# Performance work log

Measured on AMD Instinct MI355X. Metric: run time of the kernel, lower is better.

Reference implementation:

```python
import jax, jax.numpy as jnp
import numpy as np

N_NODES = 12800
N_EDGES = 204800
DIM = 16
EDGE_DIM = 4
NUM_FEAT = 3


def setup_inputs() -> dict:
    key = jax.random.key(0)
    ks = jax.random.split(key, 16)
    s = 0.1
    return {
        "x": jax.random.normal(ks[0], (N_NODES, NUM_FEAT), jnp.float32),
        "edge_index": jax.random.randint(ks[1], (2, N_EDGES), 0, N_NODES, jnp.int32),
        "edge_attr": jax.random.uniform(ks[2], (N_EDGES, EDGE_DIM), jnp.float32),
        "lin0_w": jax.random.normal(ks[3], (DIM, NUM_FEAT), jnp.float32) * s,
        "lin0_b": jax.random.normal(ks[4], (DIM,), jnp.float32) * s,
        "nn1_w": jax.random.normal(ks[5], (DIM, EDGE_DIM), jnp.float32) * s,
        "nn1_b": jax.random.normal(ks[6], (DIM,), jnp.float32) * s,
        "nn2_w": jax.random.normal(ks[7], (DIM * DIM, DIM), jnp.float32) * s,
        "nn2_b": jax.random.normal(ks[8], (DIM * DIM,), jnp.float32) * s,
        "conv_root": jax.random.normal(ks[9], (DIM, DIM), jnp.float32) * s,
        "conv_bias": jax.random.normal(ks[10], (DIM,), jnp.float32) * s,
        "gru_w_ih": jax.random.normal(ks[11], (3 * DIM, DIM), jnp.float32) * s,
        "gru_w_hh": jax.random.normal(ks[12], (3 * DIM, DIM), jnp.float32) * s,
        "gru_b_ih": jax.random.normal(ks[13], (3 * DIM,), jnp.float32) * s,
        "gru_b_hh": jax.random.normal(ks[14], (3 * DIM,), jnp.float32) * s,
    }


def _forward(x, edge_index, edge_attr, lin0_w, lin0_b, nn1_w, nn1_b, nn2_w, nn2_b,
             conv_root, conv_bias, gru_w_ih, gru_w_hh, gru_b_ih, gru_b_hh):
    n = x.shape[0]
    dim = lin0_w.shape[0]
    src, dst = edge_index[0], edge_index[1]

    # edge-conditioned weight matrices, shared across the 6 rounds: [E, dim, dim]
    e_hidden = jax.nn.relu(edge_attr @ nn1_w.T + nn1_b)
    edge_w = (e_hidden @ nn2_w.T + nn2_b).reshape(-1, dim, dim)

    # in-degree for mean aggregation (0 -> divide by 1, result stays 0)
    deg = jax.ops.segment_sum(jnp.ones_like(dst, dtype=x.dtype), dst, num_segments=n)
    inv_deg = (1.0 / jnp.maximum(deg, 1.0))[:, None]

    out = jax.nn.relu(x @ lin0_w.T + lin0_b)  # [N, dim]
    h = out
    for _ in range(6):
        # gather -> per-edge matmul -> scatter-mean
        msg = jnp.einsum('ed,edk->ek', out[src], edge_w)  # [E, dim]
        aggr = jax.ops.segment_sum(msg, dst, num_segments=n) * inv_deg
        m = jax.nn.relu(aggr + out @ conv_root + conv_bias)
        # single GRU step (seq_len = 1)
        gi = m @ gru_w_ih.T + gru_b_ih  # [N, 3*dim]
        gh = h @ gru_w_hh.T + gru_b_hh
        i_r, i_z, i_n = jnp.split(gi, 3, axis=-1)
        h_r, h_z, h_n = jnp.split(gh, 3, axis=-1)
        r = jax.nn.sigmoid(i_r + h_r)
        z = jax.nn.sigmoid(i_z + h_z)
        nhat = jnp.tanh(i_n + r * h_n)
        h = (1.0 - z) * nhat + z * h
        out = h
    return out


def reference(x, edge_index, edge_attr, lin0_w, lin0_b, nn1_w, nn1_b, nn2_w, nn2_b,
              conv_root, conv_bias, gru_w_ih, gru_w_hh, gru_b_ih, gru_b_hh):
    return _forward(x, edge_index, edge_attr, lin0_w, lin0_b, nn1_w, nn1_b, nn2_w,
                    nn2_b, conv_root, conv_bias, gru_w_ih, gru_w_hh, gru_b_ih, gru_b_hh)
```

## Files before the change

### kernel.cpp

```cpp
#include <hip/hip_runtime.h>

#define NN 12800
#define NE 204800
#define BCAP 64
#define NPB 50
#define RTHR (NPB * 16)

#define OFF_W2 0
#define OFF_CR 4416
#define OFF_WI 4736
#define OFF_WH 5696
#define OFF_CB 6656
#define OFF_BI 6672
#define OFF_BH 6720
#define PACKN  6768

__device__ __align__(16) float g_outA[NN * 16];
__device__ __align__(16) float g_outB[NN * 16];
__device__ __align__(16) float g_ehsB[NN * BCAP * 16];
__device__ __align__(16) int g_srcB[NN * BCAP];
__device__ int g_cnt[NN];
__device__ int g_perm[NN];
__device__ __align__(16) float g_wpack[PACKN];

__global__ __launch_bounds__(256) void k_setup(const int* __restrict__ ei,
                                               const float* __restrict__ x,
                                               const float* __restrict__ lw,
                                               const float* __restrict__ lb,
                                               const float* __restrict__ attr,
                                               const float* __restrict__ w1,
                                               const float* __restrict__ b1,
                                               const float* __restrict__ nn2_w,
                                               const float* __restrict__ nn2_b,
                                               const float* __restrict__ cr,
                                               const float* __restrict__ cb,
                                               const float* __restrict__ wi,
                                               const float* __restrict__ wh,
                                               const float* __restrict__ bi,
                                               const float* __restrict__ bh) {
    int gid = blockIdx.x * 256 + threadIdx.x;

    if (blockIdx.x == 0) {
        int tt = threadIdx.x;
        for (int i = tt; i < 4096; i += 256)
            g_wpack[OFF_W2 + (i & 15) * 276 + ((i >> 4) & 15) * 16 + (i >> 8)] = nn2_w[i];
        g_wpack[OFF_W2 + (tt >> 4) * 276 + 256 + (tt & 15)] = nn2_b[tt];
        g_wpack[OFF_CR + (tt & 15) * 20 + (tt >> 4)] = cr[tt];
        for (int i = tt; i < 768; i += 256) {
            g_wpack[OFF_WI + (i >> 4) * 20 + (i & 15)] = wi[i];
            g_wpack[OFF_WH + (i >> 4) * 20 + (i & 15)] = wh[i];
        }
        if (tt < 16) g_wpack[OFF_CB + tt] = cb[tt];
        if (tt < 48) { g_wpack[OFF_BI + tt] = bi[tt]; g_wpack[OFF_BH + tt] = bh[tt]; }
    }

    if (gid < NN) {
        int n = gid;
        float x0 = x[n * 3 + 0], x1 = x[n * 3 + 1], x2 = x[n * 3 + 2];
        float v[16];
#pragma unroll
        for (int j = 0; j < 16; ++j) {
            float t = lb[j] + x0 * lw[j * 3 + 0] + x1 * lw[j * 3 + 1] + x2 * lw[j * 3 + 2];
            v[j] = fmaxf(t, 0.0f);
        }
#pragma unroll
        for (int j = 0; j < 16; j += 4)
            *(float4*)(g_outA + n * 16 + j) = make_float4(v[j], v[j + 1], v[j + 2], v[j + 3]);
    }

    int e = gid;
    int s = ei[e], d = ei[NE + e];
    float4 a = *(const float4*)(attr + e * 4);
    float v[16];
#pragma unroll
    for (int j = 0; j < 16; ++j) {
        float t = b1[j] + a.x * w1[j * 4 + 0] + a.y * w1[j * 4 + 1] +
                  a.z * w1[j * 4 + 2] + a.w * w1[j * 4 + 3];
        v[j] = fmaxf(t, 0.0f);
    }
    int pos = atomicAdd(&g_cnt[d], 1);
    if (pos < BCAP) {
        int slot = d * BCAP + pos;
        g_srcB[slot] = s;
#pragma unroll
        for (int j = 0; j < 16; j += 4)
            *(float4*)(g_ehsB + slot * 16 + j) = make_float4(v[j], v[j + 1], v[j + 2], v[j + 3]);
    }
}

__global__ __launch_bounds__(1024) void k_perm() {
    __shared__ int hist[64];
    int t = threadIdx.x;
    if (t < 64) hist[t] = 0;
    __syncthreads();
    for (int n = t; n < NN; n += 1024)
        atomicAdd(&hist[min(g_cnt[n], 63)], 1);
    __syncthreads();
    if (t < 64) {
        int v = hist[t];
        int incl = v;
#pragma unroll
        for (int off = 1; off < 64; off <<= 1) {
            int u = __shfl_up(incl, off, 64);
            if (t >= off) incl += u;
        }
        hist[t] = incl - v;
    }
    __syncthreads();
    for (int n = t; n < NN; n += 1024) {
        int s = atomicAdd(&hist[min(g_cnt[n], 63)], 1);
        int blk, grp;
        if (s < 12288) {
            int c = s >> 2, r = s & 3;
            blk = c & 255;
            grp = ((c >> 8) << 2) + r;
        } else {
            int l = s - 12288;
            blk = l & 255;
            grp = 48 + (l >> 8);
        }
        g_perm[blk * NPB + grp] = n;
    }
}

__global__ __launch_bounds__(RTHR) void k_round(float* __restrict__ out_final,
                                                int flip, int last) {
    __shared__ __align__(16) float s_pack[PACKN];
    int t = threadIdx.x;
    {
        const float4* srcp = (const float4*)g_wpack;
        float4* dstp = (float4*)s_pack;
        for (int idx = t; idx < PACKN / 4; idx += RTHR) dstp[idx] = srcp[idx];
    }
    __syncthreads();

    const float* s_W2  = s_pack + OFF_W2;
    const float* s_crT = s_pack + OFF_CR;
    const float* s_wi  = s_pack + OFF_WI;
    const float* s_wh  = s_pack + OFF_WH;
    const float* s_cb  = s_pack + OFF_CB;
    const float* s_bi  = s_pack + OFF_BI;
    const float* s_bh  = s_pack + OFF_BH;

    const float* cur = flip ? g_outB : g_outA;
    float*       nxt = flip ? g_outA : g_outB;

    const int grp = t >> 4, j = t & 15;
    const int n = min(max(g_perm[blockIdx.x * NPB + grp], 0), NN - 1);
    int deg = min(g_cnt[n], BCAP);
    if (last && j == 0) g_cnt[n] = 0;
    const int base = n * BCAP;

    float Gd[16];
#pragma unroll
    for (int d = 0; d < 16; ++d) Gd[d] = 0.0f;
    float r16 = 0.0f;
#pragma unroll 4
    for (int q = 0; q < deg; ++q) {
        int slot = base + q;
        int s = min(g_srcB[slot], NN - 1);
        const float* orow = cur + s * 16;
        float ej = g_ehsB[slot * 16 + j];
        float4 o0 = *(const float4*)(orow + 0);
        float4 o1 = *(const float4*)(orow + 4);
        float4 o2 = *(const float4*)(orow + 8);
        float4 o3 = *(const float4*)(orow + 12);
        Gd[0]  += ej * o0.x; Gd[1]  += ej * o0.y; Gd[2]  += ej * o0.z; Gd[3]  += ej * o0.w;
        Gd[4]  += ej * o1.x; Gd[5]  += ej * o1.y; Gd[6]  += ej * o1.z; Gd[7]  += ej * o1.w;
        Gd[8]  += ej * o2.x; Gd[9]  += ej * o2.y; Gd[10] += ej * o2.z; Gd[11] += ej * o2.w;
        Gd[12] += ej * o3.x; Gd[13] += ej * o3.y; Gd[14] += ej * o3.z; Gd[15] += ej * o3.w;
        r16 += orow[j];
    }

    const float* wj = s_W2 + j * 276;
    float part[16];
#pragma unroll
    for (int kp = 0; kp < 16; ++kp) {
        const float* w = wj + kp * 16;
        float4 w0 = *(const float4*)(w + 0);
        float4 w1 = *(const float4*)(w + 4);
        float4 w2 = *(const float4*)(w + 8);
        float4 w3 = *(const float4*)(w + 12);
        part[kp] = Gd[0] * w0.x + Gd[1] * w0.y + Gd[2] * w0.z + Gd[3] * w0.w
                 + Gd[4] * w1.x + Gd[5] * w1.y + Gd[6] * w1.z + Gd[7] * w1.w
                 + Gd[8] * w2.x + Gd[9] * w2.y + Gd[10] * w2.z + Gd[11] * w2.w
                 + Gd[12] * w3.x + Gd[13] * w3.y + Gd[14] * w3.z + Gd[15] * w3.w;
    }
    {
        float4 b0 = *(const float4*)(wj + 256);
        float4 b1 = *(const float4*)(wj + 260);
        float4 b2v = *(const float4*)(wj + 264);
        float4 b3 = *(const float4*)(wj + 268);
        part[0] += r16 * b0.x;  part[1] += r16 * b0.y;  part[2] += r16 * b0.z;  part[3] += r16 * b0.w;
        part[4] += r16 * b1.x;  part[5] += r16 * b1.y;  part[6] += r16 * b1.z;  part[7] += r16 * b1.w;
        part[8] += r16 * b2v.x; part[9] += r16 * b2v.y; part[10] += r16 * b2v.z; part[11] += r16 * b2v.w;
        part[12] += r16 * b3.x; part[13] += r16 * b3.y; part[14] += r16 * b3.z; part[15] += r16 * b3.w;
    }

    float w8[8];
#pragma unroll
    for (int i = 0; i < 8; ++i) {
        int keep = 2 * i + (j & 1);
        w8[i] = part[keep] + __shfl_xor(part[keep ^ 1], 1);
    }
    float w4[4];
#pragma unroll
    for (int i = 0; i < 4; ++i) {
        int keep = 2 * i + ((j >> 1) & 1);
        w4[i] = w8[keep] + __shfl_xor(w8[keep ^ 1], 2);
    }
    float w2[2];
#pragma unroll
    for (int i = 0; i < 2; ++i) {
        int keep = 2 * i + ((j >> 2) & 1);
        w2[i] = w4[keep] + __shfl_xor(w4[keep ^ 1], 4);
    }
    float aggr;
    {
        int keep = (j >> 3) & 1;
        aggr = w2[keep] + __shfl_xor(w2[keep ^ 1], 8);
    }
    float invd = 1.0f / (float)(deg > 0 ? deg : 1);
    float a_k = aggr * invd;
    const int k = j;

    const float* nrow = cur + n * 16;
    float4 q0 = *(const float4*)(nrow + 0);
    float4 q1 = *(const float4*)(nrow + 4);
    float4 q2 = *(const float4*)(nrow + 8);
    float4 q3 = *(const float4*)(nrow + 12);
    float o[16] = {q0.x, q0.y, q0.z, q0.w, q1.x, q1.y, q1.z, q1.w,
                   q2.x, q2.y, q2.z, q2.w, q3.x, q3.y, q3.z, q3.w};
    float ok = o[k];

    float mcc = s_cb[k] + a_k;
    {
        const float* c = s_crT + k * 20;
        float4 c0 = *(const float4*)(c + 0);
        float4 c1 = *(const float4*)(c + 4);
        float4 c2 = *(const float4*)(c + 8);
        float4 c3 = *(const float4*)(c + 12);
        mcc += o[0] * c0.x + o[1] * c0.y + o[2] * c0.z + o[3] * c0.w
             + o[4] * c1.x + o[5] * c1.y + o[6] * c1.z + o[7] * c1.w
             + o[8] * c2.x + o[9] * c2.y + o[10] * c2.z + o[11] * c2.w
             + o[12] * c3.x + o[13] * c3.y + o[14] * c3.z + o[15] * c3.w;
    }
    float m = fmaxf(mcc, 0.0f);

    float md[16];
#pragma unroll
    for (int d = 0; d < 16; ++d) md[d] = __shfl(m, d, 16);

    float ir = s_bi[k], iz = s_bi[16 + k], in_ = s_bi[32 + k];
    float hr = s_bh[k], hz = s_bh[16 + k], hh = s_bh[32 + k];
#pragma unroll
    for (int g = 0; g < 3; ++g) {
        const float* wrow_i = s_wi + (g * 16 + k) * 20;
        const float* wrow_h = s_wh + (g * 16 + k) * 20;
        float acc_i = 0.0f, acc_h = 0.0f;
#pragma unroll
        for (int d4 = 0; d4 < 4; ++d4) {
            float4 wiv = *(const float4*)(wrow_i + d4 * 4);
            float4 whv = *(const float4*)(wrow_h + d4 * 4);
            acc_i += md[d4 * 4] * wiv.x + md[d4 * 4 + 1] * wiv.y
                   + md[d4 * 4 + 2] * wiv.z + md[d4 * 4 + 3] * wiv.w;
            acc_h += o[d4 * 4] * whv.x + o[d4 * 4 + 1] * whv.y
                   + o[d4 * 4 + 2] * whv.z + o[d4 * 4 + 3] * whv.w;
        }
        if (g == 0) { ir += acc_i; hr += acc_h; }
        else if (g == 1) { iz += acc_i; hz += acc_h; }
        else { in_ += acc_i; hh += acc_h; }
    }
    float rg = 1.0f / (1.0f + __expf(-(ir + hr)));
    float z  = 1.0f / (1.0f + __expf(-(iz + hz)));
    float nh = tanhf(in_ + rg * hh);
    float hnew = (1.0f - z) * nh + z * ok;

    if (last) out_final[n * 16 + k] = hnew;
    else      nxt[n * 16 + k] = hnew;
}

extern "C" void kernel_launch(void* const* d_in, const int* in_sizes, int n_in,
                              void* d_out, int out_size, void* d_ws, size_t ws_size,
                              hipStream_t stream) {
    const float* x         = (const float*)d_in[0];
    const int*   ei        = (const int*)d_in[1];
    const float* edge_attr = (const float*)d_in[2];
    const float* lin0_w    = (const float*)d_in[3];
    const float* lin0_b    = (const float*)d_in[4];
    const float* nn1_w     = (const float*)d_in[5];
    const float* nn1_b     = (const float*)d_in[6];
    const float* nn2_w     = (const float*)d_in[7];
    const float* nn2_b     = (const float*)d_in[8];
    const float* conv_root = (const float*)d_in[9];
    const float* conv_bias = (const float*)d_in[10];
    const float* gru_w_ih  = (const float*)d_in[11];
    const float* gru_w_hh  = (const float*)d_in[12];
    const float* gru_b_ih  = (const float*)d_in[13];
    const float* gru_b_hh  = (const float*)d_in[14];
    float* out = (float*)d_out;

    k_setup<<<NE / 256, 256, 0, stream>>>(ei, x, lin0_w, lin0_b, edge_attr,
                                          nn1_w, nn1_b, nn2_w, nn2_b, conv_root,
                                          conv_bias, gru_w_ih, gru_w_hh,
                                          gru_b_ih, gru_b_hh);
    k_perm<<<1, 1024, 0, stream>>>();

    for (int r = 0; r < 6; ++r) {
        k_round<<<NN / NPB, RTHR, 0, stream>>>(out, r & 1, r == 5 ? 1 : 0);
    }
}
```

Measured before the change: 235.8 us.

## Assign one full wavefront per node, splitting edges across four subgroups

Each node now gets a 64-lane wavefront instead of a 16-lane group. The four 16-lane subgroups each take every fourth incoming edge, and their partial sums are combined with cross-lane shuffles. The W2 contraction is also split across subgroups, so each lane computes 4 outputs instead of 16, and the permutation now deals degree-sorted nodes round-robin across blocks. This targets latency in the serial per-edge gather loop and register pressure, at the cost of four times as many threads, extra shuffles, and redundant GRU work in lanes 16-63, which do not write results.

```diff
diff --git a/kernel.cpp b/kernel.cpp
--- a/kernel.cpp
+++ b/kernel.cpp
@@ -4,7 +4,9 @@
 #define NE 204800
 #define BCAP 64
 #define NPB 50
-#define RTHR (NPB * 16)
+#define BTHR 512
+#define WPB 8
+#define NBLK2 (NN / WPB)
 
 #define OFF_W2 0
 #define OFF_CR 4416
@@ -109,28 +111,20 @@
     __syncthreads();
     for (int n = t; n < NN; n += 1024) {
         int s = atomicAdd(&hist[min(g_cnt[n], 63)], 1);
-        int blk, grp;
-        if (s < 12288) {
-            int c = s >> 2, r = s & 3;
-            blk = c & 255;
-            grp = ((c >> 8) << 2) + r;
-        } else {
-            int l = s - 12288;
-            blk = l & 255;
-            grp = 48 + (l >> 8);
-        }
-        g_perm[blk * NPB + grp] = n;
+        int blk = s % NBLK2;
+        int wv  = s / NBLK2;
+        g_perm[blk * WPB + wv] = n;
     }
 }
 
-__global__ __launch_bounds__(RTHR) void k_round(float* __restrict__ out_final,
+__global__ __launch_bounds__(BTHR) void k_round(float* __restrict__ out_final,
                                                 int flip, int last) {
     __shared__ __align__(16) float s_pack[PACKN];
     int t = threadIdx.x;
     {
         const float4* srcp = (const float4*)g_wpack;
         float4* dstp = (float4*)s_pack;
-        for (int idx = t; idx < PACKN / 4; idx += RTHR) dstp[idx] = srcp[idx];
+        for (int idx = t; idx < PACKN / 4; idx += BTHR) dstp[idx] = srcp[idx];
     }
     __syncthreads();
 
@@ -145,97 +139,100 @@
     const float* cur = flip ? g_outB : g_outA;
     float*       nxt = flip ? g_outA : g_outB;
 
-    const int grp = t >> 4, j = t & 15;
-    const int n = min(max(g_perm[blockIdx.x * NPB + grp], 0), NN - 1);
+    const int wave = t >> 6, lane = t & 63;
+    const int sg = lane >> 4, j = lane & 15;
+    const int n = min(max(g_perm[blockIdx.x * WPB + wave], 0), NN - 1);
     int deg = min(g_cnt[n], BCAP);
-    if (last && j == 0) g_cnt[n] = 0;
+    if (last && lane == 0) g_cnt[n] = 0;
     const int base = n * BCAP;
+
+    int sB = min(max(g_srcB[base + lane], 0), NN - 1);
 
     float Gd[16];
 #pragma unroll
     for (int d = 0; d < 16; ++d) Gd[d] = 0.0f;
     float r16 = 0.0f;
-#pragma unroll 4
-    for (int q = 0; q < deg; ++q) {
-        int slot = base + q;
-        int s = min(g_srcB[slot], NN - 1);
-        const float* orow = cur + s * 16;
-        float ej = g_ehsB[slot * 16 + j];
-        float4 o0 = *(const float4*)(orow + 0);
-        float4 o1 = *(const float4*)(orow + 4);
-        float4 o2 = *(const float4*)(orow + 8);
-        float4 o3 = *(const float4*)(orow + 12);
-        Gd[0]  += ej * o0.x; Gd[1]  += ej * o0.y; Gd[2]  += ej * o0.z; Gd[3]  += ej * o0.w;
-        Gd[4]  += ej * o1.x; Gd[5]  += ej * o1.y; Gd[6]  += ej * o1.z; Gd[7]  += ej * o1.w;
-        Gd[8]  += ej * o2.x; Gd[9]  += ej * o2.y; Gd[10] += ej * o2.z; Gd[11] += ej * o2.w;
-        Gd[12] += ej * o3.x; Gd[13] += ej * o3.y; Gd[14] += ej * o3.z; Gd[15] += ej * o3.w;
-        r16 += orow[j];
-    }
+
+    for (int i = 0; i < 16; ++i) {
+        if (4 * i >= deg) break;
+        int q = 4 * i + sg;
+        int s = __shfl(sB, q, 64);
+        if (q < deg) {
+            const float* orow = cur + s * 16;
+            float ej = g_ehsB[(base + q) * 16 + j];
+            float4 o0 = *(const float4*)(orow + 0);
+            float4 o1 = *(const float4*)(orow + 4);
+            float4 o2 = *(const float4*)(orow + 8);
+            float4 o3 = *(const float4*)(orow + 12);
+            Gd[0]  += ej * o0.x; Gd[1]  += ej * o0.y; Gd[2]  += ej * o0.z; Gd[3]  += ej * o0.w;
+            Gd[4]  += ej * o1.x; Gd[5]  += ej * o1.y; Gd[6]  += ej * o1.z; Gd[7]  += ej * o1.w;
+            Gd[8]  += ej * o2.x; Gd[9]  += ej * o2.y; Gd[10] += ej * o2.z; Gd[11] += ej * o2.w;
+            Gd[12] += ej * o3.x; Gd[13] += ej * o3.y; Gd[14] += ej * o3.z; Gd[15] += ej * o3.w;
+            r16 += orow[j];
+        }
+    }
+
+#pragma unroll
+    for (int d = 0; d < 16; ++d) {
+        Gd[d] += __shfl_xor(Gd[d], 16);
+        Gd[d] += __shfl_xor(Gd[d], 32);
+    }
+    r16 += __shfl_xor(r16, 16);
+    r16 += __shfl_xor(r16, 32);
 
     const float* wj = s_W2 + j * 276;
-    float part[16];
-#pragma unroll
-    for (int kp = 0; kp < 16; ++kp) {
-        const float* w = wj + kp * 16;
+    float part[4];
+#pragma unroll
+    for (int m = 0; m < 4; ++m) {
+        const float* w = wj + (4 * m + sg) * 16;
         float4 w0 = *(const float4*)(w + 0);
         float4 w1 = *(const float4*)(w + 4);
         float4 w2 = *(const float4*)(w + 8);
         float4 w3 = *(const float4*)(w + 12);
-        part[kp] = Gd[0] * w0.x + Gd[1] * w0.y + Gd[2] * w0.z + Gd[3] * w0.w
-                 + Gd[4] * w1.x + Gd[5] * w1.y + Gd[6] * w1.z + Gd[7] * w1.w
-                 + Gd[8] * w2.x + Gd[9] * w2.y + Gd[10] * w2.z + Gd[11] * w2.w
-                 + Gd[12] * w3.x + Gd[13] * w3.y + Gd[14] * w3.z + Gd[15] * w3.w;
-    }
+        part[m] = Gd[0] * w0.x + Gd[1] * w0.y + Gd[2] * w0.z + Gd[3] * w0.w
+                + Gd[4] * w1.x + Gd[5] * w1.y + Gd[6] * w1.z + Gd[7] * w1.w
+                + Gd[8] * w2.x + Gd[9] * w2.y + Gd[10] * w2.z + Gd[11] * w2.w
+                + Gd[12] * w3.x + Gd[13] * w3.y + Gd[14] * w3.z + Gd[15] * w3.w;
+        part[m] += r16 * wj[256 + 4 * m + sg];
+    }
+
+    const bool sel0 = (j & 1) != 0;
+    const bool sel1 = ((j >> 1) & 1) != 0;
+    float w2v[2];
+#pragma unroll
+    for (int i = 0; i < 2; ++i) {
+        float a = part[2 * i], b = part[2 * i + 1];
+        float keepv = sel0 ? b : a;
+        float othv  = sel0 ? a : b;
+        w2v[i] = keepv + __shfl_xor(othv, 1);
+    }
+    float vsum;
     {
-        float4 b0 = *(const float4*)(wj + 256);
-        float4 b1 = *(const float4*)(wj + 260);
-        float4 b2v = *(const float4*)(wj + 264);
-        float4 b3 = *(const float4*)(wj + 268);
-        part[0] += r16 * b0.x;  part[1] += r16 * b0.y;  part[2] += r16 * b0.z;  part[3] += r16 * b0.w;
-        part[4] += r16 * b1.x;  part[5] += r16 * b1.y;  part[6] += r16 * b1.z;  part[7] += r16 * b1.w;
-        part[8] += r16 * b2v.x; part[9] += r16 * b2v.y; part[10] += r16 * b2v.z; part[11] += r16 * b2v.w;
-        part[12] += r16 * b3.x; part[13] += r16 * b3.y; part[14] += r16 * b3.z; part[15] += r16 * b3.w;
-    }
-
-    float w8[8];
-#pragma unroll
-    for (int i = 0; i < 8; ++i) {
-        int keep = 2 * i + (j & 1);
-        w8[i] = part[keep] + __shfl_xor(part[keep ^ 1], 1);
-    }
-    float w4[4];
-#pragma unroll
-    for (int i = 0; i < 4; ++i) {
-        int keep = 2 * i + ((j >> 1) & 1);
-        w4[i] = w8[keep] + __shfl_xor(w8[keep ^ 1], 2);
-    }
-    float w2[2];
-#pragma unroll
-    for (int i = 0; i < 2; ++i) {
-        int keep = 2 * i + ((j >> 2) & 1);
-        w2[i] = w4[keep] + __shfl_xor(w4[keep ^ 1], 4);
-    }
-    float aggr;
-    {
-        int keep = (j >> 3) & 1;
-        aggr = w2[keep] + __shfl_xor(w2[keep ^ 1], 8);
-    }
+        float a = w2v[0], b = w2v[1];
+        float keepv = sel1 ? b : a;
+        float othv  = sel1 ? a : b;
+        vsum = keepv + __shfl_xor(othv, 2);
+    }
+    vsum += __shfl_xor(vsum, 4);
+    vsum += __shfl_xor(vsum, 8);
+
+    const int kk = lane & 15;
+    float aggr = __shfl(vsum, ((kk & 3) << 4) | (kk >> 2), 64);
     float invd = 1.0f / (float)(deg > 0 ? deg : 1);
     float a_k = aggr * invd;
-    const int k = j;
 
     const float* nrow = cur + n * 16;
-    float4 q0 = *(const float4*)(nrow + 0);
-    float4 q1 = *(const float4*)(nrow + 4);
-    float4 q2 = *(const float4*)(nrow + 8);
-    float4 q3 = *(const float4*)(nrow + 12);
-    float o[16] = {q0.x, q0.y, q0.z, q0.w, q1.x, q1.y, q1.z, q1.w,
-                   q2.x, q2.y, q2.z, q2.w, q3.x, q3.y, q3.z, q3.w};
-    float ok = o[k];
-
-    float mcc = s_cb[k] + a_k;
+    float4 q0v = *(const float4*)(nrow + 0);
+    float4 q1v = *(const float4*)(nrow + 4);
+    float4 q2v = *(const float4*)(nrow + 8);
+    float4 q3v = *(const float4*)(nrow + 12);
+    float o[16] = {q0v.x, q0v.y, q0v.z, q0v.w, q1v.x, q1v.y, q1v.z, q1v.w,
+                   q2v.x, q2v.y, q2v.z, q2v.w, q3v.x, q3v.y, q3v.z, q3v.w};
+    float ok = nrow[kk];
+
+    float mcc = s_cb[kk] + a_k;
     {
-        const float* c = s_crT + k * 20;
+        const float* c = s_crT + kk * 20;
         float4 c0 = *(const float4*)(c + 0);
         float4 c1 = *(const float4*)(c + 4);
         float4 c2 = *(const float4*)(c + 8);
@@ -251,12 +248,12 @@
 #pragma unroll
     for (int d = 0; d < 16; ++d) md[d] = __shfl(m, d, 16);
 
-    float ir = s_bi[k], iz = s_bi[16 + k], in_ = s_bi[32 + k];
-    float hr = s_bh[k], hz = s_bh[16 + k], hh = s_bh[32 + k];
+    float ir = s_bi[kk], iz = s_bi[16 + kk], in_ = s_bi[32 + kk];
+    float hr = s_bh[kk], hz = s_bh[16 + kk], hh = s_bh[32 + kk];
 #pragma unroll
     for (int g = 0; g < 3; ++g) {
-        const float* wrow_i = s_wi + (g * 16 + k) * 20;
-        const float* wrow_h = s_wh + (g * 16 + k) * 20;
+        const float* wrow_i = s_wi + (g * 16 + kk) * 20;
+        const float* wrow_h = s_wh + (g * 16 + kk) * 20;
         float acc_i = 0.0f, acc_h = 0.0f;
 #pragma unroll
         for (int d4 = 0; d4 < 4; ++d4) {
@@ -276,8 +273,10 @@
     float nh = tanhf(in_ + rg * hh);
     float hnew = (1.0f - z) * nh + z * ok;
 
-    if (last) out_final[n * 16 + k] = hnew;
-    else      nxt[n * 16 + k] = hnew;
+    if (lane < 16) {
+        if (last) out_final[n * 16 + kk] = hnew;
+        else      nxt[n * 16 + kk] = hnew;
+    }
 }
 
 extern "C" void kernel_launch(void* const* d_in, const int* in_sizes, int n_in,
@@ -307,6 +306,6 @@
     k_perm<<<1, 1024, 0, stream>>>();
 
     for (int r = 0; r < 6; ++r) {
-        k_round<<<NN / NPB, RTHR, 0, stream>>>(out, r & 1, r == 5 ? 1 : 0);
+        k_round<<<NBLK2, BTHR, 0, stream>>>(out, r & 1, r == 5 ? 1 : 0);
     }
 }
```

After: 287.8 us. 22.1% more time.

## Use 32 lanes per node splitting edges across two half-groups

Applied to the files above, without the earlier changes.

Each node is now processed by 32 threads instead of 16, with the two 16-lane halves taking alternating edges and merging partial accumulators through shuffles. Source indices are preloaded once per lane and broadcast with shuffles instead of being reloaded serially, and the W2 contraction and reduction tree are split across the halves. The permutation is remapped to 512 blocks of 25 nodes. The aim is to halve the serial per-edge latency chain and raise memory-level parallelism, at the cost of more shuffles and a duplicated GRU tail in which half of the lanes do redundant work.

```diff
diff --git a/kernel.cpp b/kernel.cpp
--- a/kernel.cpp
+++ b/kernel.cpp
@@ -3,8 +3,9 @@
 #define NN 12800
 #define NE 204800
 #define BCAP 64
-#define NPB 50
-#define RTHR (NPB * 16)
+#define RTHR 800
+#define NPB2 25
+#define NBLK2 (NN / NPB2)
 
 #define OFF_W2 0
 #define OFF_CR 4416
@@ -111,15 +112,15 @@
         int s = atomicAdd(&hist[min(g_cnt[n], 63)], 1);
         int blk, grp;
         if (s < 12288) {
-            int c = s >> 2, r = s & 3;
-            blk = c & 255;
-            grp = ((c >> 8) << 2) + r;
+            int c = s >> 1;
+            blk = c & 511;
+            grp = ((c >> 9) << 1) + (s & 1);
         } else {
             int l = s - 12288;
-            blk = l & 255;
-            grp = 48 + (l >> 8);
-        }
-        g_perm[blk * NPB + grp] = n;
+            blk = l & 511;
+            grp = 24;
+        }
+        g_perm[blk * NPB2 + grp] = n;
     }
 }
 
@@ -145,81 +146,92 @@
     const float* cur = flip ? g_outB : g_outA;
     float*       nxt = flip ? g_outA : g_outB;
 
-    const int grp = t >> 4, j = t & 15;
-    const int n = min(max(g_perm[blockIdx.x * NPB + grp], 0), NN - 1);
+    const int grp = t >> 5;
+    const int l   = t & 31;
+    const int sub = l >> 4, j = l & 15;
+    const int n = min(max(g_perm[blockIdx.x * NPB2 + grp], 0), NN - 1);
     int deg = min(g_cnt[n], BCAP);
-    if (last && j == 0) g_cnt[n] = 0;
+    if (last && l == 0) g_cnt[n] = 0;
     const int base = n * BCAP;
+
+    int s0 = min(max(g_srcB[base + l], 0), NN - 1);
+    int s1 = min(max(g_srcB[base + 32 + l], 0), NN - 1);
 
     float Gd[16];
 #pragma unroll
     for (int d = 0; d < 16; ++d) Gd[d] = 0.0f;
     float r16 = 0.0f;
+
 #pragma unroll 4
-    for (int q = 0; q < deg; ++q) {
-        int slot = base + q;
-        int s = min(g_srcB[slot], NN - 1);
-        const float* orow = cur + s * 16;
-        float ej = g_ehsB[slot * 16 + j];
-        float4 o0 = *(const float4*)(orow + 0);
-        float4 o1 = *(const float4*)(orow + 4);
-        float4 o2 = *(const float4*)(orow + 8);
-        float4 o3 = *(const float4*)(orow + 12);
-        Gd[0]  += ej * o0.x; Gd[1]  += ej * o0.y; Gd[2]  += ej * o0.z; Gd[3]  += ej * o0.w;
-        Gd[4]  += ej * o1.x; Gd[5]  += ej * o1.y; Gd[6]  += ej * o1.z; Gd[7]  += ej * o1.w;
-        Gd[8]  += ej * o2.x; Gd[9]  += ej * o2.y; Gd[10] += ej * o2.z; Gd[11] += ej * o2.w;
-        Gd[12] += ej * o3.x; Gd[13] += ej * o3.y; Gd[14] += ej * o3.z; Gd[15] += ej * o3.w;
-        r16 += orow[j];
-    }
+    for (int i = 0; i < 32; ++i) {
+        if (2 * i >= deg) break;
+        int q = 2 * i + sub;
+        int sv = (2 * i < 32) ? __shfl(s0, q & 31, 32) : __shfl(s1, q & 31, 32);
+        if (q < deg) {
+            const float* orow = cur + sv * 16;
+            float ej = g_ehsB[(base + q) * 16 + j];
+            float4 o0 = *(const float4*)(orow + 0);
+            float4 o1 = *(const float4*)(orow + 4);
+            float4 o2 = *(const float4*)(orow + 8);
+            float4 o3 = *(const float4*)(orow + 12);
+            Gd[0]  += ej * o0.x; Gd[1]  += ej * o0.y; Gd[2]  += ej * o0.z; Gd[3]  += ej * o0.w;
+            Gd[4]  += ej * o1.x; Gd[5]  += ej * o1.y; Gd[6]  += ej * o1.z; Gd[7]  += ej * o1.w;
+            Gd[8]  += ej * o2.x; Gd[9]  += ej * o2.y; Gd[10] += ej * o2.z; Gd[11] += ej * o2.w;
+            Gd[12] += ej * o3.x; Gd[13] += ej * o3.y; Gd[14] += ej * o3.z; Gd[15] += ej * o3.w;
+            r16 += orow[j];
+        }
+    }
+
+#pragma unroll
+    for (int d = 0; d < 16; ++d) Gd[d] += __shfl_xor(Gd[d], 16);
+    r16 += __shfl_xor(r16, 16);
 
     const float* wj = s_W2 + j * 276;
-    float part[16];
-#pragma unroll
-    for (int kp = 0; kp < 16; ++kp) {
-        const float* w = wj + kp * 16;
+    float part[8];
+#pragma unroll
+    for (int m = 0; m < 8; ++m) {
+        const float* w = wj + (2 * m + sub) * 16;
         float4 w0 = *(const float4*)(w + 0);
         float4 w1 = *(const float4*)(w + 4);
         float4 w2 = *(const float4*)(w + 8);
         float4 w3 = *(const float4*)(w + 12);
-        part[kp] = Gd[0] * w0.x + Gd[1] * w0.y + Gd[2] * w0.z + Gd[3] * w0.w
-                 + Gd[4] * w1.x + Gd[5] * w1.y + Gd[6] * w1.z + Gd[7] * w1.w
-                 + Gd[8] * w2.x + Gd[9] * w2.y + Gd[10] * w2.z + Gd[11] * w2.w
-                 + Gd[12] * w3.x + Gd[13] * w3.y + Gd[14] * w3.z + Gd[15] * w3.w;
-    }
+        part[m] = Gd[0] * w0.x + Gd[1] * w0.y + Gd[2] * w0.z + Gd[3] * w0.w
+                + Gd[4] * w1.x + Gd[5] * w1.y + Gd[6] * w1.z + Gd[7] * w1.w
+                + Gd[8] * w2.x + Gd[9] * w2.y + Gd[10] * w2.z + Gd[11] * w2.w
+                + Gd[12] * w3.x + Gd[13] * w3.y + Gd[14] * w3.z + Gd[15] * w3.w;
+        part[m] += r16 * wj[256 + 2 * m + sub];
+    }
+
+    const bool sel0 = (j & 1) != 0;
+    const bool sel1 = ((j >> 1) & 1) != 0;
+    const bool sel2 = ((j >> 2) & 1) != 0;
+
+    float e4[4];
+#pragma unroll
+    for (int i = 0; i < 4; ++i) {
+        float a = part[2 * i], b = part[2 * i + 1];
+        float keepv = sel0 ? b : a;
+        float othv  = sel0 ? a : b;
+        e4[i] = keepv + __shfl_xor(othv, 1);
+    }
+    float e2[2];
+#pragma unroll
+    for (int i = 0; i < 2; ++i) {
+        float a = e4[2 * i], b = e4[2 * i + 1];
+        float keepv = sel1 ? b : a;
+        float othv  = sel1 ? a : b;
+        e2[i] = keepv + __shfl_xor(othv, 2);
+    }
+    float e1;
     {
-        float4 b0 = *(const float4*)(wj + 256);
-        float4 b1 = *(const float4*)(wj + 260);
-        float4 b2v = *(const float4*)(wj + 264);
-        float4 b3 = *(const float4*)(wj + 268);
-        part[0] += r16 * b0.x;  part[1] += r16 * b0.y;  part[2] += r16 * b0.z;  part[3] += r16 * b0.w;
-        part[4] += r16 * b1.x;  part[5] += r16 * b1.y;  part[6] += r16 * b1.z;  part[7] += r16 * b1.w;
-        part[8] += r16 * b2v.x; part[9] += r16 * b2v.y; part[10] += r16 * b2v.z; part[11] += r16 * b2v.w;
-        part[12] += r16 * b3.x; part[13] += r16 * b3.y; part[14] += r16 * b3.z; part[15] += r16 * b3.w;
-    }
-
-    float w8[8];
-#pragma unroll
-    for (int i = 0; i < 8; ++i) {
-        int keep = 2 * i + (j & 1);
-        w8[i] = part[keep] + __shfl_xor(part[keep ^ 1], 1);
-    }
-    float w4[4];
-#pragma unroll
-    for (int i = 0; i < 4; ++i) {
-        int keep = 2 * i + ((j >> 1) & 1);
-        w4[i] = w8[keep] + __shfl_xor(w8[keep ^ 1], 2);
-    }
-    float w2[2];
-#pragma unroll
-    for (int i = 0; i < 2; ++i) {
-        int keep = 2 * i + ((j >> 2) & 1);
-        w2[i] = w4[keep] + __shfl_xor(w4[keep ^ 1], 4);
-    }
-    float aggr;
-    {
-        int keep = (j >> 3) & 1;
-        aggr = w2[keep] + __shfl_xor(w2[keep ^ 1], 8);
-    }
+        float a = e2[0], b = e2[1];
+        float keepv = sel2 ? b : a;
+        float othv  = sel2 ? a : b;
+        e1 = keepv + __shfl_xor(othv, 4);
+    }
+    float vsum = e1 + __shfl_xor(e1, 8);
+
+    float aggr = __shfl(vsum, ((j & 1) << 4) | (j >> 1), 32);
     float invd = 1.0f / (float)(deg > 0 ? deg : 1);
     float a_k = aggr * invd;
     const int k = j;
@@ -231,7 +243,7 @@
     float4 q3 = *(const float4*)(nrow + 12);
     float o[16] = {q0.x, q0.y, q0.z, q0.w, q1.x, q1.y, q1.z, q1.w,
                    q2.x, q2.y, q2.z, q2.w, q3.x, q3.y, q3.z, q3.w};
-    float ok = o[k];
+    float ok = nrow[k];
 
     float mcc = s_cb[k] + a_k;
     {
@@ -276,8 +288,10 @@
     float nh = tanhf(in_ + rg * hh);
     float hnew = (1.0f - z) * nh + z * ok;
 
-    if (last) out_final[n * 16 + k] = hnew;
-    else      nxt[n * 16 + k] = hnew;
+    if (sub == 0) {
+        if (last) out_final[n * 16 + k] = hnew;
+        else      nxt[n * 16 + k] = hnew;
+    }
 }
 
 extern "C" void kernel_launch(void* const* d_in, const int* in_sizes, int n_in,
@@ -307,6 +321,6 @@
     k_perm<<<1, 1024, 0, stream>>>();
 
     for (int r = 0; r < 6; ++r) {
-        k_round<<<NN / NPB, RTHR, 0, stream>>>(out, r & 1, r == 5 ? 1 : 0);
+        k_round<<<NBLK2, RTHR, 0, stream>>>(out, r & 1, r == 5 ? 1 : 0);
     }
 }
```

Measured after the change: 238.5 us. No clear change (+1.2%).
